# Kernel tuning notes

Hardware: AMD Instinct MI355X
Metric: run time of the kernel (lower is better)

The kernel has to match this reference:

```python
import jax, jax.numpy as jnp
import numpy as np

EPS = 1e-08


def setup_inputs() -> dict:
    key = jax.random.key(0)
    k1, k2, k3 = jax.random.split(key, 3)
    B, T, IN, OUT = 32, 500, 2048, 1024
    x = jax.random.normal(k1, (B, T, IN), dtype=jnp.float32)
    # torch init: normal(mean=0, std=w_init_std*sqrt(1/input_shape))
    w = jax.random.normal(k2, (IN, OUT), dtype=jnp.float32) * np.sqrt(1.0 / IN)
    # b ~ N(1.0, 0.01), clamped >= 0
    b = jnp.clip(1.0 + 0.01 * jax.random.normal(k3, (OUT,), dtype=jnp.float32), 0.0, None)
    decay_m = jnp.array([0.6], dtype=jnp.float32)  # N(0.6, .01) clamped to [0,1]
    decay_s = jnp.array([0.9], dtype=jnp.float32)  # N(0.9, .01) clamped to [0,1]
    return {"x": x, "w": w, "b": b, "decay_m": decay_m, "decay_s": decay_s}


def reference(x, w, b, decay_m, decay_s):
    # x: [B, T, IN]; w: [IN, OUT]
    B, T, _ = x.shape
    OUT = w.shape[1]
    h = jnp.einsum('btc,cd->btd', x, w)          # [B, T, OUT]
    norm = jnp.sum(w * w, axis=0)                 # [OUT]
    dm = decay_m[0]
    ds = decay_s[0]
    inv_norm = 1.0 / (norm + EPS)
    zeros = jnp.zeros((B, OUT), dtype=x.dtype)
    # spk is never assigned a spike value in the original forward (spike_fn
    # is never applied), so it remains zero throughout.
    spk = zeros

    def step(carry, inp):
        M, S, E = carry
        E = dm * norm * (E + spk)                 # spk == 0 (faithful to source)
        M = dm * (M + inp)
        S = ds * (S + inp)
        mem = M - S - E
        mthr = mem * inv_norm - b                 # [B, OUT]
        return (M, S, E), mthr

    (_, _, _), spk_rec_t = jax.lax.scan(step, (zeros, zeros, zeros),
                                        jnp.swapaxes(h, 0, 1))  # [T, B, OUT]
    spk_rec = jnp.swapaxes(spk_rec_t, 0, 1)       # [B, T, OUT]
    loss = 0.5 * jnp.mean(spk_rec ** 2)
    return (spk_rec, loss)
```

## Files before the change

kernel.cpp:

```cpp
#include <hip/hip_runtime.h>


typedef __bf16 bf16x8 __attribute__((ext_vector_type(8)));
typedef __bf16 bf16x4 __attribute__((ext_vector_type(4)));
typedef float  f32x4  __attribute__((ext_vector_type(4)));

#define BDIM 32
#define TDIM 500
#define INDIM 2048
#define OUTDIM 1024
#define MROWS 16000
#define NCHUNK 25
#define CHLEN 20
#define OUT_ELEMS 16384000

__device__ __forceinline__ void gld_lds16(const void* g, void* l) {
    __builtin_amdgcn_global_load_lds(
        (const __attribute__((address_space(1))) unsigned int*)g,
        (__attribute__((address_space(3))) unsigned int*)l, 16, 0, 0);
}

__global__ void convert_x(const float* __restrict__ x, __bf16* __restrict__ xb) {
    size_t i = ((size_t)blockIdx.x * 256 + threadIdx.x) * 8;
    float4 a = *(const float4*)(x + i);
    float4 b = *(const float4*)(x + i + 4);
    bf16x8 o;
    o[0] = (__bf16)a.x; o[1] = (__bf16)a.y; o[2] = (__bf16)a.z; o[3] = (__bf16)a.w;
    o[4] = (__bf16)b.x; o[5] = (__bf16)b.y; o[6] = (__bf16)b.z; o[7] = (__bf16)b.w;
    *(bf16x8*)(xb + i) = o;
}

__global__ void transpose_w(const float* __restrict__ w, __bf16* __restrict__ wbt,
                            float* __restrict__ normAcc) {
    __shared__ float tile[32][33];
    __shared__ float red[8][33];
    const int tx = threadIdx.x;
    const int ty = threadIdx.y;
    const int d0 = blockIdx.x * 32;
    const int c0 = blockIdx.y * 32;
    float s = 0.f;
#pragma unroll
    for (int i = 0; i < 4; ++i) {
        int c = c0 + ty + i * 8;
        float v = w[(size_t)c * OUTDIM + d0 + tx];
        tile[ty + i * 8][tx] = v;
        s += v * v;
    }
    red[ty][tx] = s;
    __syncthreads();
#pragma unroll
    for (int i = 0; i < 4; ++i) {
        int d = d0 + ty + i * 8;
        wbt[(size_t)d * INDIM + c0 + tx] = (__bf16)tile[tx][ty + i * 8];
    }
    if (ty == 0) {
        float t = red[0][tx] + red[1][tx] + red[2][tx] + red[3][tx]
                + red[4][tx] + red[5][tx] + red[6][tx] + red[7][tx];
        atomicAdd(&normAcc[d0 + tx], t);
    }
}

__global__ __launch_bounds__(512, 2) void gemm_bf16(
    const __bf16* __restrict__ A,
    const __bf16* __restrict__ Bt,
    __bf16* __restrict__ H)
{
    constexpr int K  = INDIM;
    constexpr int NT = K / 32;
    __shared__ __align__(16) __bf16 As[4][256 * 32];
    __shared__ __align__(16) __bf16 Bs[4][256 * 32];

    const int tid  = threadIdx.x;
    const int wave = tid >> 6;
    const int lane = tid & 63;
    const int wm   = wave >> 2;
    const int wn   = wave & 3;

    const int orig = blockIdx.x;
    const int xcd = orig & 7, within = orig >> 3;
    const int wgid = (xcd < 4) ? (xcd * 32 + within)
                               : (128 + (xcd - 4) * 31 + within);
    const int bm = (wgid >> 2) * 256;
    const int bn = (wgid & 3) * 256;

    const int srow = lane >> 2;
    const int sseg = lane & 3;
    const int scol = (sseg ^ ((srow >> 1) & 3)) * 8;
    const int lds0 = (wave * 16) * 32;
    const int lds1 = (128 + wave * 16) * 32;
    int rA0 = bm +       wave * 16 + srow; if (rA0 > MROWS - 1) rA0 = MROWS - 1;
    int rA1 = bm + 128 + wave * 16 + srow; if (rA1 > MROWS - 1) rA1 = MROWS - 1;
    const __bf16* gA0 = A  + (size_t)rA0 * K + scol;
    const __bf16* gA1 = A  + (size_t)rA1 * K + scol;
    const __bf16* gB0 = Bt + (size_t)(bn +       wave * 16 + srow) * K + scol;
    const __bf16* gB1 = Bt + (size_t)(bn + 128 + wave * 16 + srow) * K + scol;

    const int mrow = lane & 15, quad = lane >> 4;
    const int swzq = quad ^ ((mrow >> 1) & 3);
    const int rdA = (wm * 128 + mrow) * 32 + swzq * 8;
    const int rdB = (wn * 64  + mrow) * 32 + swzq * 8;

    f32x4 acc[8][4] = {};

#define STAGE(tt) do { const int _b = (tt) & 3; const size_t _k = (size_t)(tt) * 32; \
        gld_lds16(gA0 + _k, &As[_b][lds0]);                                          \
        gld_lds16(gA1 + _k, &As[_b][lds1]);                                          \
        gld_lds16(gB0 + _k, &Bs[_b][lds0]);                                          \
        gld_lds16(gB1 + _k, &Bs[_b][lds1]); } while (0)

    STAGE(0); STAGE(1); STAGE(2); STAGE(3);
    asm volatile("s_waitcnt vmcnt(12)" ::: "memory");
    asm volatile("s_barrier" ::: "memory");

#pragma unroll 1
    for (int t = 0; t < NT; ++t) {
        const __bf16* as = As[t & 3];
        const __bf16* bs = Bs[t & 3];
        bf16x8 af[4], bfr[4];
#pragma unroll
        for (int i = 0; i < 4; ++i) af[i]  = *(const bf16x8*)&as[rdA + i * 512];
#pragma unroll
        for (int j = 0; j < 4; ++j) bfr[j] = *(const bf16x8*)&bs[rdB + j * 512];
        asm volatile("s_barrier" ::: "memory");
        __builtin_amdgcn_s_setprio(1);
#pragma unroll
        for (int i = 0; i < 4; ++i)
#pragma unroll
            for (int j = 0; j < 4; ++j)
                acc[i][j] = __builtin_amdgcn_mfma_f32_16x16x32_bf16(
                    af[i], bfr[j], acc[i][j], 0, 0, 0);
        __builtin_amdgcn_s_setprio(0);
        asm volatile("s_barrier" ::: "memory");
#pragma unroll
        for (int i = 0; i < 4; ++i) af[i] = *(const bf16x8*)&as[rdA + 2048 + i * 512];
        asm volatile("s_barrier" ::: "memory");
        __builtin_amdgcn_s_setprio(1);
#pragma unroll
        for (int i = 0; i < 4; ++i)
#pragma unroll
            for (int j = 0; j < 4; ++j)
                acc[4 + i][j] = __builtin_amdgcn_mfma_f32_16x16x32_bf16(
                    af[i], bfr[j], acc[4 + i][j], 0, 0, 0);
        __builtin_amdgcn_s_setprio(0);
        asm volatile("s_barrier" ::: "memory");
        if (t + 4 < NT) STAGE(t + 4);
        if (t < NT - 4)       asm volatile("s_waitcnt vmcnt(12)" ::: "memory");
        else if (t == NT - 4) asm volatile("s_waitcnt vmcnt(8)"  ::: "memory");
        else if (t == NT - 3) asm volatile("s_waitcnt vmcnt(4)"  ::: "memory");
        else if (t == NT - 2) asm volatile("s_waitcnt vmcnt(0)"  ::: "memory");
        if (t < NT - 1) asm volatile("s_barrier" ::: "memory");
    }
#undef STAGE

    const int Rb = bm + wm * 128 + quad * 4;
    const int Cb = bn + wn * 64 + mrow;
#pragma unroll
    for (int i = 0; i < 8; ++i)
#pragma unroll
        for (int j = 0; j < 4; ++j)
#pragma unroll
            for (int r = 0; r < 4; ++r) {
                const int R = Rb + i * 16 + r;
                if (R < MROWS)
                    H[(size_t)R * OUTDIM + Cb + j * 16] = (__bf16)acc[i][j][r];
            }
}

__global__ void scan1(const __bf16* __restrict__ H,
                      f32x4* __restrict__ cM, f32x4* __restrict__ cS,
                      const float* __restrict__ dmp, const float* __restrict__ dsp) {
    const float dm = *dmp, ds = *dsp;
    const int c = blockIdx.x, b = blockIdx.y, tid = threadIdx.x;
    f32x4 M = {}, S = {};
    const __bf16* p = H + ((size_t)b * TDIM + c * CHLEN) * OUTDIM + tid * 4;
#pragma unroll 4
    for (int t = 0; t < CHLEN; ++t) {
        bf16x4 hv = *(const bf16x4*)(p + (size_t)t * OUTDIM);
        f32x4 h; h[0] = hv[0]; h[1] = hv[1]; h[2] = hv[2]; h[3] = hv[3];
        M = dm * (M + h);
        S = ds * (S + h);
    }
    const size_t idx = ((size_t)c * BDIM + b) * 256 + tid;
    cM[idx] = M;
    cS[idx] = S;
}

__global__ void scan2(float* __restrict__ cM, float* __restrict__ cS,
                      const float* __restrict__ dmp, const float* __restrict__ dsp) {
    const float dm = *dmp, ds = *dsp;
    float km = 1.f, ks = 1.f;
#pragma unroll
    for (int i = 0; i < CHLEN; ++i) { km *= dm; ks *= ds; }
    const int gid = blockIdx.x * 256 + threadIdx.x;
    const int b = gid >> 10, d = gid & 1023;
    float tM = 0.f, tS = 0.f;
    for (int c = 0; c < NCHUNK; ++c) {
        const size_t idx = (((size_t)c * BDIM + b) << 10) + d;
        float oM = cM[idx], oS = cS[idx];
        cM[idx] = tM; cS[idx] = tS;
        tM = km * tM + oM;
        tS = ks * tS + oS;
    }
}

__global__ void scan3(const __bf16* __restrict__ H,
                      const f32x4* __restrict__ cM, const f32x4* __restrict__ cS,
                      const float* __restrict__ normAcc, const float* __restrict__ bias,
                      const float* __restrict__ dmp, const float* __restrict__ dsp,
                      float* __restrict__ out, float* __restrict__ lossAcc,
                      unsigned* __restrict__ ticket) {
    const float dm = *dmp, ds = *dsp;
    const int c = blockIdx.x, b = blockIdx.y, tid = threadIdx.x;
    const size_t cidx = ((size_t)c * BDIM + b) * 256 + tid;
    f32x4 M = cM[cidx];
    f32x4 S = cS[cidx];
    f32x4 nv = *(const f32x4*)(normAcc + tid * 4);
    f32x4 inv;
    inv[0] = 1.f / (nv[0] + 1e-8f); inv[1] = 1.f / (nv[1] + 1e-8f);
    inv[2] = 1.f / (nv[2] + 1e-8f); inv[3] = 1.f / (nv[3] + 1e-8f);
    f32x4 bv = *(const f32x4*)(bias + tid * 4);

    const size_t rowbase = ((size_t)b * TDIM + c * CHLEN) * OUTDIM + tid * 4;
    const __bf16* p = H + rowbase;
    float* o = out + rowbase;
    float loss = 0.f;
#pragma unroll 4
    for (int t = 0; t < CHLEN; ++t) {
        bf16x4 hv = *(const bf16x4*)(p + (size_t)t * OUTDIM);
        f32x4 h; h[0] = hv[0]; h[1] = hv[1]; h[2] = hv[2]; h[3] = hv[3];
        M = dm * (M + h);
        S = ds * (S + h);
        f32x4 r = (M - S) * inv - bv;
        *(f32x4*)(o + (size_t)t * OUTDIM) = r;
        loss += r[0] * r[0] + r[1] * r[1] + r[2] * r[2] + r[3] * r[3];
    }
    __shared__ float red[256];
    red[tid] = loss;
    __syncthreads();
    for (int s = 128; s > 0; s >>= 1) {
        if (tid < s) red[tid] += red[tid + s];
        __syncthreads();
    }
    if (tid == 0) {
        atomicAdd(lossAcc, red[0]);
        __threadfence();
        unsigned t = atomicAdd(ticket, 1u);
        if (t == NCHUNK * BDIM - 1) {
            float total = atomicAdd(lossAcc, 0.0f);
            out[OUT_ELEMS] = 0.5f * total / (float)OUT_ELEMS;
        }
    }
}

#define OFF_H      ((size_t)0)
#define OFF_WBT    ((size_t)32768000)
#define OFF_NORM   ((size_t)36962304)
#define OFF_LOSS   ((size_t)36966400)
#define OFF_TICKET ((size_t)36966404)
#define OFF_CM     ((size_t)36966656)
#define OFF_CS     ((size_t)40243456)

extern "C" void kernel_launch(void* const* d_in, const int* in_sizes, int n_in,
                              void* d_out, int out_size, void* d_ws, size_t ws_size,
                              hipStream_t stream) {
    const float* x  = (const float*)d_in[0];
    const float* w  = (const float*)d_in[1];
    const float* bb = (const float*)d_in[2];
    const float* dm = (const float*)d_in[3];
    const float* ds = (const float*)d_in[4];

    char* ws = (char*)d_ws;
    __bf16*   H    = (__bf16*)(ws + OFF_H);
    __bf16*   WBT  = (__bf16*)(ws + OFF_WBT);
    float*    NORM = (float*)(ws + OFF_NORM);
    float*    LOSS = (float*)(ws + OFF_LOSS);
    unsigned* TICK = (unsigned*)(ws + OFF_TICKET);
    f32x4*    CM   = (f32x4*)(ws + OFF_CM);
    f32x4*    CS   = (f32x4*)(ws + OFF_CS);
    __bf16*   XB   = (__bf16*)d_out;
    float*    out  = (float*)d_out;

    hipMemsetAsync(ws + OFF_NORM, 0, 4096 + 256, stream);

    convert_x<<<16000, 256, 0, stream>>>(x, XB);
    transpose_w<<<dim3(32, 64), dim3(32, 8), 0, stream>>>(w, WBT, NORM);
    gemm_bf16<<<252, 512, 0, stream>>>(XB, WBT, H);
    scan1<<<dim3(NCHUNK, BDIM), 256, 0, stream>>>(H, CM, CS, dm, ds);
    scan2<<<128, 256, 0, stream>>>((float*)CM, (float*)CS, dm, ds);
    scan3<<<dim3(NCHUNK, BDIM), 256, 0, stream>>>(H, CM, CS, NORM, bb, dm, ds,
                                                  out, LOSS, TICK);
}
```

Baseline: 361.4 us.

## Retile GEMM to 256x128 blocks with 3-stage LDS ring and fragment prefetch

```diff
diff --git a/kernel.cpp b/kernel.cpp
--- a/kernel.cpp
+++ b/kernel.cpp
@@ -60,40 +60,45 @@
     }
 }
 
-__global__ __launch_bounds__(512, 2) void gemm_bf16(
+__global__ __launch_bounds__(256, 2) void gemm_bf16(
     const __bf16* __restrict__ A,
     const __bf16* __restrict__ Bt,
     __bf16* __restrict__ H)
 {
     constexpr int K  = INDIM;
     constexpr int NT = K / 32;
-    __shared__ __align__(16) __bf16 As[4][256 * 32];
-    __shared__ __align__(16) __bf16 Bs[4][256 * 32];
+    __shared__ __align__(16) __bf16 As[3][256 * 32];
+    __shared__ __align__(16) __bf16 Bs[3][128 * 32];
 
     const int tid  = threadIdx.x;
     const int wave = tid >> 6;
     const int lane = tid & 63;
-    const int wm   = wave >> 2;
-    const int wn   = wave & 3;
+    const int wm   = wave >> 1;
+    const int wn   = wave & 1;
 
     const int orig = blockIdx.x;
-    const int xcd = orig & 7, within = orig >> 3;
-    const int wgid = (xcd < 4) ? (xcd * 32 + within)
-                               : (128 + (xcd - 4) * 31 + within);
-    const int bm = (wgid >> 2) * 256;
-    const int bn = (wgid & 3) * 256;
+    const int wgid = (orig & 7) * 63 + (orig >> 3);
+    const int bm = (wgid >> 3) * 256;
+    const int bn = (wgid & 7) * 128;
 
     const int srow = lane >> 2;
     const int sseg = lane & 3;
     const int scol = (sseg ^ ((srow >> 1) & 3)) * 8;
-    const int lds0 = (wave * 16) * 32;
-    const int lds1 = (128 + wave * 16) * 32;
-    int rA0 = bm +       wave * 16 + srow; if (rA0 > MROWS - 1) rA0 = MROWS - 1;
-    int rA1 = bm + 128 + wave * 16 + srow; if (rA1 > MROWS - 1) rA1 = MROWS - 1;
-    const __bf16* gA0 = A  + (size_t)rA0 * K + scol;
-    const __bf16* gA1 = A  + (size_t)rA1 * K + scol;
-    const __bf16* gB0 = Bt + (size_t)(bn +       wave * 16 + srow) * K + scol;
-    const __bf16* gB1 = Bt + (size_t)(bn + 128 + wave * 16 + srow) * K + scol;
+    const __bf16* gA[4]; int ldsA[4];
+#pragma unroll
+    for (int g = 0; g < 4; ++g) {
+        const int q = wave * 4 + g;
+        int r = bm + q * 16 + srow; if (r > MROWS - 1) r = MROWS - 1;
+        gA[g]  = A + (size_t)r * K + scol;
+        ldsA[g] = q * 16 * 32;
+    }
+    const __bf16* gB[2]; int ldsB[2];
+#pragma unroll
+    for (int g = 0; g < 2; ++g) {
+        const int p = wave * 2 + g;
+        gB[g]  = Bt + (size_t)(bn + p * 16 + srow) * K + scol;
+        ldsB[g] = p * 16 * 32;
+    }
 
     const int mrow = lane & 15, quad = lane >> 4;
     const int swzq = quad ^ ((mrow >> 1) & 3);
@@ -101,56 +106,71 @@
     const int rdB = (wn * 64  + mrow) * 32 + swzq * 8;
 
     f32x4 acc[8][4] = {};
-
-#define STAGE(tt) do { const int _b = (tt) & 3; const size_t _k = (size_t)(tt) * 32; \
-        gld_lds16(gA0 + _k, &As[_b][lds0]);                                          \
-        gld_lds16(gA1 + _k, &As[_b][lds1]);                                          \
-        gld_lds16(gB0 + _k, &Bs[_b][lds0]);                                          \
-        gld_lds16(gB1 + _k, &Bs[_b][lds1]); } while (0)
-
-    STAGE(0); STAGE(1); STAGE(2); STAGE(3);
+    int ib = 0;
+
+    auto stage = [&](int tt, __bf16* as, __bf16* bs) {
+        const size_t k = (size_t)tt * 32;
+#pragma unroll
+        for (int g = 0; g < 4; ++g) gld_lds16(gA[g] + k, as + ldsA[g]);
+#pragma unroll
+        for (int g = 0; g < 2; ++g) gld_lds16(gB[g] + k, bs + ldsB[g]);
+    };
+
+    stage(0, &As[0][0], &Bs[0][0]);
+    stage(1, &As[1][0], &Bs[1][0]);
+    stage(2, &As[2][0], &Bs[2][0]);
     asm volatile("s_waitcnt vmcnt(12)" ::: "memory");
     asm volatile("s_barrier" ::: "memory");
 
-#pragma unroll 1
-    for (int t = 0; t < NT; ++t) {
-        const __bf16* as = As[t & 3];
-        const __bf16* bs = Bs[t & 3];
-        bf16x8 af[4], bfr[4];
-#pragma unroll
-        for (int i = 0; i < 4; ++i) af[i]  = *(const bf16x8*)&as[rdA + i * 512];
-#pragma unroll
-        for (int j = 0; j < 4; ++j) bfr[j] = *(const bf16x8*)&bs[rdB + j * 512];
-        asm volatile("s_barrier" ::: "memory");
-        __builtin_amdgcn_s_setprio(1);
+    bf16x8 afA[4], bfA[4], afB[4], bfB[4];
+    {
+        const __bf16* as = &As[0][0]; const __bf16* bs = &Bs[0][0];
+#pragma unroll
+        for (int j = 0; j < 4; ++j) bfA[j] = *(const bf16x8*)&bs[rdB + j * 512];
+#pragma unroll
+        for (int i = 0; i < 4; ++i) afA[i] = *(const bf16x8*)&as[rdA + i * 512];
+    }
+
+    auto iter = [&](int T, bf16x8 (&afC)[4], bf16x8 (&bfC)[4],
+                           bf16x8 (&afN)[4], bf16x8 (&bfN)[4]) {
+        const __bf16* as = &As[ib][0];
+        bf16x8 af1[4];
+#pragma unroll
+        for (int i = 0; i < 4; ++i) af1[i] = *(const bf16x8*)&as[rdA + 2048 + i * 512];
 #pragma unroll
         for (int i = 0; i < 4; ++i)
 #pragma unroll
             for (int j = 0; j < 4; ++j)
                 acc[i][j] = __builtin_amdgcn_mfma_f32_16x16x32_bf16(
-                    af[i], bfr[j], acc[i][j], 0, 0, 0);
-        __builtin_amdgcn_s_setprio(0);
+                    afC[i], bfC[j], acc[i][j], 0, 0, 0);
+        asm volatile("s_waitcnt lgkmcnt(0)" ::: "memory");
         asm volatile("s_barrier" ::: "memory");
-#pragma unroll
-        for (int i = 0; i < 4; ++i) af[i] = *(const bf16x8*)&as[rdA + 2048 + i * 512];
-        asm volatile("s_barrier" ::: "memory");
-        __builtin_amdgcn_s_setprio(1);
+        if (T + 3 < NT) stage(T + 3, &As[ib][0], &Bs[ib][0]);
+        if (T < NT - 3)      asm volatile("s_waitcnt vmcnt(12)" ::: "memory");
+        else if (T == NT - 3) asm volatile("s_waitcnt vmcnt(6)" ::: "memory");
+        else if (T == NT - 2) asm volatile("s_waitcnt vmcnt(0)" ::: "memory");
+        ib = (ib == 2) ? 0 : ib + 1;
+        if (T < NT - 1) {
+            asm volatile("s_barrier" ::: "memory");
+            const __bf16* asn = &As[ib][0]; const __bf16* bsn = &Bs[ib][0];
+#pragma unroll
+            for (int j = 0; j < 4; ++j) bfN[j] = *(const bf16x8*)&bsn[rdB + j * 512];
+#pragma unroll
+            for (int i = 0; i < 4; ++i) afN[i] = *(const bf16x8*)&asn[rdA + i * 512];
+        }
 #pragma unroll
         for (int i = 0; i < 4; ++i)
 #pragma unroll
             for (int j = 0; j < 4; ++j)
                 acc[4 + i][j] = __builtin_amdgcn_mfma_f32_16x16x32_bf16(
-                    af[i], bfr[j], acc[4 + i][j], 0, 0, 0);
-        __builtin_amdgcn_s_setprio(0);
-        asm volatile("s_barrier" ::: "memory");
-        if (t + 4 < NT) STAGE(t + 4);
-        if (t < NT - 4)       asm volatile("s_waitcnt vmcnt(12)" ::: "memory");
-        else if (t == NT - 4) asm volatile("s_waitcnt vmcnt(8)"  ::: "memory");
-        else if (t == NT - 3) asm volatile("s_waitcnt vmcnt(4)"  ::: "memory");
-        else if (t == NT - 2) asm volatile("s_waitcnt vmcnt(0)"  ::: "memory");
-        if (t < NT - 1) asm volatile("s_barrier" ::: "memory");
-    }
-#undef STAGE
+                    af1[i], bfC[j], acc[4 + i][j], 0, 0, 0);
+    };
+
+#pragma unroll 1
+    for (int t = 0; t < NT; t += 2) {
+        iter(t,     afA, bfA, afB, bfB);
+        iter(t + 1, afB, bfB, afA, bfA);
+    }
 
     const int Rb = bm + wm * 128 + quad * 4;
     const int Cb = bn + wn * 64 + mrow;
@@ -284,7 +304,7 @@
 
     convert_x<<<16000, 256, 0, stream>>>(x, XB);
     transpose_w<<<dim3(32, 64), dim3(32, 8), 0, stream>>>(w, WBT, NORM);
-    gemm_bf16<<<252, 512, 0, stream>>>(XB, WBT, H);
+    gemm_bf16<<<504, 256, 0, stream>>>(XB, WBT, H);
     scan1<<<dim3(NCHUNK, BDIM), 256, 0, stream>>>(H, CM, CS, dm, ds);
     scan2<<<128, 256, 0, stream>>>((float*)CM, (float*)CS, dm, ds);
     scan3<<<dim3(NCHUNK, BDIM), 256, 0, stream>>>(H, CM, CS, NORM, bb, dm, ds,
```

After: 341.4 us. 5.5% less time.
